# Optimization experiments

Measured on AMD Instinct MI355X. Metric: run time of the kernel, lower is better.

## Reference

```python
import math
import jax, jax.numpy as jnp
import numpy as np

MAX_LEN = 1024

def _sinusoidal_pe(seq_len, d_model):
    pos = jnp.arange(seq_len, dtype=jnp.float32)[:, None]
    div = jnp.exp(jnp.arange(0, d_model, 2, dtype=jnp.float32) * (-math.log(10000.0) / d_model))
    ang = pos * div  # [S, D/2]
    pe = jnp.zeros((seq_len, d_model), dtype=jnp.float32)
    pe = pe.at[:, 0::2].set(jnp.sin(ang))
    pe = pe.at[:, 1::2].set(jnp.cos(ang))
    return pe

def setup_inputs() -> dict:
    key = jax.random.key(0)
    ks = jax.random.split(key, 4)
    B, S, D, H = 4, 1024, 1024, 16
    x = jax.random.normal(ks[0], (B, S, D), dtype=jnp.float32)
    gamma = jnp.ones((D,), dtype=jnp.float32)
    beta = jnp.zeros((D,), dtype=jnp.float32)
    w_pos = jax.random.normal(ks[1], (2 * D, D), dtype=jnp.float32) * (1.0 / math.sqrt(D))
    w_tok = jax.random.normal(ks[2], (3 * D, D), dtype=jnp.float32) * (1.0 / math.sqrt(D))
    bias_table = jax.random.normal(ks[3], (2 * MAX_LEN, H), dtype=jnp.float32) * 0.02
    return {"x": x, "gamma": gamma, "beta": beta, "w_pos": w_pos, "w_tok": w_tok, "bias_table": bias_table}

def reference(x, gamma, beta, w_pos, w_tok, bias_table):
    B, S, D = x.shape
    H = bias_table.shape[1]
    dh = D // H
    scale = 1.0 / math.sqrt(2 * dh)

    # untied positional scores (identical across batch)
    pe = _sinusoidal_pe(S, D)                      # [S, D]
    pos = pe @ w_pos.T                             # [S, 2D]
    pos_k, pos_q = pos[:, :D], pos[:, D:]
    pos_k = pos_k.reshape(S, H, dh)
    pos_q = pos_q.reshape(S, H, dh)
    pos_attn = jnp.einsum('qhd,khd->hqk', pos_q, pos_k)  # [H, S, S]

    # token scores
    mu = jnp.mean(x, axis=-1, keepdims=True)
    var = jnp.mean((x - mu) ** 2, axis=-1, keepdims=True)
    xn = (x - mu) / jnp.sqrt(var + 1e-5) * gamma + beta
    tok = xn @ w_tok.T                             # [B, S, 3D]
    tok_k, tok_q, tok_v = jnp.split(tok, 3, axis=-1)
    tok_k = tok_k.reshape(B, S, H, dh)
    tok_q = tok_q.reshape(B, S, H, dh)
    tok_v = tok_v.reshape(B, S, H, dh)
    tok_attn = jnp.einsum('bqhd,bkhd->bhqk', tok_q, tok_k)  # [B, H, S, S]

    attn = (tok_attn + pos_attn[None]) / scale

    # relative-position bias
    rel = jnp.arange(S)[None, :] - jnp.arange(S)[:, None] + MAX_LEN  # [S, S]
    bias = bias_table[rel]                         # [S, S, H]
    attn = attn + jnp.transpose(bias, (2, 0, 1))[None]

    attn = jax.nn.softmax(attn, axis=-1)
    out = jnp.einsum('bhqk,bkhd->bqhd', attn, tok_v)
    return out.reshape(B, S, D)
```

## Files before the change

kernel.cpp:

```cpp
#include <hip/hip_runtime.h>
#include <math.h>

#define SB 1024
#define DM 1024
#define BB 4
#define NH 16
#define DH 64
#define ML 1024

typedef __attribute__((ext_vector_type(8))) short short8;
typedef __attribute__((ext_vector_type(8))) _Float16 half8;
typedef __attribute__((ext_vector_type(4))) float f32x4;
typedef unsigned short u16;

__device__ __forceinline__ u16 f2bf(float x) {
  unsigned u = __float_as_uint(x);
  u += 0x7fffu + ((u >> 16) & 1u);
  return (u16)(u >> 16);
}
__device__ __forceinline__ float bf2f(u16 h) { return __uint_as_float((unsigned)h << 16); }

__device__ __forceinline__ void async16(void* lds, const void* g) {
  __builtin_amdgcn_global_load_lds(
      (const __attribute__((address_space(1))) unsigned*)g,
      (__attribute__((address_space(3))) unsigned*)lds, 16, 0, 0);
}

#define TPITCH 1028

__global__ __launch_bounds__(256, 4) void prep_all(
    const float* __restrict__ x, const float* __restrict__ gamma,
    const float* __restrict__ beta,
    const float* __restrict__ w_pos, const float* __restrict__ w_tok,
    _Float16* __restrict__ peH, _Float16* __restrict__ peL,
    _Float16* __restrict__ xnH, _Float16* __restrict__ xnL,
    _Float16* __restrict__ wpH, _Float16* __restrict__ wpL,
    _Float16* __restrict__ wtH, _Float16* __restrict__ wtL) {
  __shared__ float T[8 * TPITCH];
  __shared__ float Sred[4][8][2];

  int bid = blockIdx.x, t = threadIdx.x;
  int wv = t >> 6, lane = t & 63;

  int type, rt;
  const float* src = nullptr;
  _Float16 *dH, *dL;
  if (bid < 128)      { type = 0; rt = bid;       dH = peH; dL = peL; }
  else if (bid < 640) { type = 1; rt = bid - 128; src = x;     dH = xnH; dL = xnL; }
  else if (bid < 896) { type = 2; rt = bid - 640; src = w_pos; dH = wpH; dL = wpL; }
  else                { type = 2; rt = bid - 896; src = w_tok; dH = wtH; dL = wtL; }

  if (type == 0) {
    float div0 = exp2f((float)(t * 4)     * (-0.01297628162065376f));
    float div1 = exp2f((float)(t * 4 + 2) * (-0.01297628162065376f));
    #pragma unroll
    for (int i = 0; i < 8; ++i) {
      float p = (float)(rt * 8 + i);
      float a0 = p * div0, a1 = p * div1;
      float4 f;
      f.x = __sinf(a0); f.y = __cosf(a0);
      f.z = __sinf(a1); f.w = __cosf(a1);
      *(float4*)&T[i * TPITCH + t * 4] = f;
    }
  } else if (type == 1) {
    #pragma unroll
    for (int i = 0; i < 8; ++i) {
      float4 f = *(const float4*)(src + (size_t)(rt * 8 + i) * 1024 + t * 4);
      *(float4*)&T[i * TPITCH + t * 4] = f;
    }
  } else {
    #pragma unroll
    for (int i = 0; i < 8; ++i) {
      float4 f = *(const float4*)(src + (size_t)(rt * 8 + i) * 1024 + t * 4);
      f.x *= 32.f; f.y *= 32.f; f.z *= 32.f; f.w *= 32.f;
      *(float4*)&T[i * TPITCH + t * 4] = f;
    }
  }
  __syncthreads();

  if (type == 1) {
    int row = t & 7, cc = t >> 3;
    float s1 = 0.f, s2 = 0.f;
    #pragma unroll
    for (int i = 0; i < 8; ++i) {
      float4 f = *(const float4*)&T[row * TPITCH + cc * 32 + i * 4];
      s1 += f.x + f.y + f.z + f.w;
      s2 += f.x*f.x + f.y*f.y + f.z*f.z + f.w*f.w;
    }
    s1 += __shfl_xor(s1, 8, 64);  s2 += __shfl_xor(s2, 8, 64);
    s1 += __shfl_xor(s1, 16, 64); s2 += __shfl_xor(s2, 16, 64);
    s1 += __shfl_xor(s1, 32, 64); s2 += __shfl_xor(s2, 32, 64);
    if (lane < 8) { Sred[wv][lane][0] = s1; Sred[wv][lane][1] = s2; }
  }
  __syncthreads();

  int row = lane & 7, gg = (lane >> 3) & 3, ktp = lane >> 5;
  float mu = 0.f, rs = 0.f;
  if (type == 1) {
    float s1 = Sred[0][row][0] + Sred[1][row][0] + Sred[2][row][0] + Sred[3][row][0];
    float s2 = Sred[0][row][1] + Sred[1][row][1] + Sred[2][row][1] + Sred[3][row][1];
    mu = s1 * (1.0f / 1024.0f);
    float var = s2 * (1.0f / 1024.0f) - mu * mu;
    rs = rsqrtf(var + 1e-5f);
  }
  int grow16 = rt >> 1;
  int rsub = (rt & 1) * 8 + row;
  #pragma unroll
  for (int q = 0; q < 4; ++q) {
    int kt = wv * 8 + q * 2 + ktp;
    int col = kt * 32 + gg * 8;
    float v[8];
    *(float4*)&v[0] = *(const float4*)&T[row * TPITCH + col];
    *(float4*)&v[4] = *(const float4*)&T[row * TPITCH + col + 4];
    if (type == 1) {
      float4 gp0 = *(const float4*)(gamma + col);
      float4 gp1 = *(const float4*)(gamma + col + 4);
      float4 bp0 = *(const float4*)(beta + col);
      float4 bp1 = *(const float4*)(beta + col + 4);
      v[0] = (v[0]-mu)*rs*gp0.x + bp0.x;  v[1] = (v[1]-mu)*rs*gp0.y + bp0.y;
      v[2] = (v[2]-mu)*rs*gp0.z + bp0.z;  v[3] = (v[3]-mu)*rs*gp0.w + bp0.w;
      v[4] = (v[4]-mu)*rs*gp1.x + bp1.x;  v[5] = (v[5]-mu)*rs*gp1.y + bp1.y;
      v[6] = (v[6]-mu)*rs*gp1.z + bp1.z;  v[7] = (v[7]-mu)*rs*gp1.w + bp1.w;
    }
    half8 hv, lv;
    #pragma unroll
    for (int j = 0; j < 8; ++j) {
      _Float16 h = (_Float16)v[j];
      hv[j] = h;
      lv[j] = (_Float16)(v[j] - (float)h);
    }
    size_t off = ((size_t)(grow16 * 32 + kt) * 64 + rsub + gg * 16) * 8;
    *(half8*)(dH + off) = hv;
    *(half8*)(dL + off) = lv;
  }
}

__global__ __launch_bounds__(256, 2) void gemm16p(
    const _Float16* __restrict__ AtH, const _Float16* __restrict__ AtL,
    const _Float16* __restrict__ ApH, const _Float16* __restrict__ ApL,
    const _Float16* __restrict__ BtH, const _Float16* __restrict__ BtL,
    const _Float16* __restrict__ BpH, const _Float16* __restrict__ BpL,
    u16* __restrict__ KtfH, u16* __restrict__ KtfL,
    u16* __restrict__ KpfH, u16* __restrict__ KpfL,
    u16* __restrict__ QH, u16* __restrict__ QL,
    u16* __restrict__ pQH, u16* __restrict__ pQL,
    u16* __restrict__ vF, float sK, float sQ, float sV) {
  __shared__ _Float16 L[32 * 512];
  int t = threadIdx.x;
  int wv = t >> 6, lane = t & 63;
  int wm = wv >> 1, wn = wv & 1;
  int r16 = lane & 15, g = lane >> 4;

  int phys = blockIdx.x;
  int bid = (phys & 7) * 56 + (phys >> 3);
  bool isPos = (bid >= 384);
  int idx = isPos ? bid - 384 : bid;
  int n0, m0;
  const _Float16 *AH, *AL, *BH, *BL;
  if (isPos) { n0 = (idx & 7) * 256;  m0 = (idx >> 3) * 128;
               AH = ApH; AL = ApL; BH = BpH; BL = BpL; }
  else       { n0 = (idx % 12) * 256; m0 = (idx / 12) * 128;
               AH = AtH; AL = AtL; BH = BtH; BL = BtL; }
  int mt0 = m0 >> 4, nt0 = n0 >> 4;
  bool split = isPos || (n0 < 2048);

  f32x4 acc[4][8];
  #pragma unroll
  for (int i = 0; i < 4; ++i)
    #pragma unroll
    for (int j = 0; j < 8; ++j) acc[i][j] = (f32x4){0.f, 0.f, 0.f, 0.f};

  for (int kt = 0; kt < 32; ++kt) {
    __syncthreads();
    #pragma unroll
    for (int rd = 0; rd < 8; ++rd) {
      int ci = rd * 4 + wv;
      bool isAlo = (ci < 16) && (ci & 1);
      if (!split && isAlo) continue;
      const _Float16* src;
      if (ci < 16) {
        int mt = ci >> 1, pl = ci & 1;
        const _Float16* P = pl ? AL : AH;
        src = P + ((size_t)((mt0 + mt) * 32 + kt) * 64 + lane) * 8;
      } else {
        int nt = ci - 16;
        src = BH + ((size_t)((nt0 + nt) * 32 + kt) * 64 + lane) * 8;
      }
      async16(&L[ci * 512], src);
    }
    half8 blo[8];
    if (split) {
      #pragma unroll
      for (int j = 0; j < 8; ++j) {
        int ntg = nt0 + wn * 8 + j;
        blo[j] = *(const half8*)(BL + ((size_t)(ntg * 32 + kt) * 64 + lane) * 8);
      }
    }
    __syncthreads();

    half8 ah[4], al[4];
    #pragma unroll
    for (int i = 0; i < 4; ++i)
      ah[i] = *(const half8*)&L[(((wm * 4 + i) * 2 + 0) * 512) + lane * 8];
    if (split) {
      #pragma unroll
      for (int i = 0; i < 4; ++i)
        al[i] = *(const half8*)&L[(((wm * 4 + i) * 2 + 1) * 512) + lane * 8];
    }
    #pragma unroll
    for (int j = 0; j < 8; ++j) {
      half8 bh = *(const half8*)&L[((16 + wn * 8 + j) * 512) + lane * 8];
      #pragma unroll
      for (int i = 0; i < 4; ++i) {
        acc[i][j] = __builtin_amdgcn_mfma_f32_16x16x32_f16(ah[i], bh, acc[i][j], 0, 0, 0);
        if (split) {
          acc[i][j] = __builtin_amdgcn_mfma_f32_16x16x32_f16(al[i], bh, acc[i][j], 0, 0, 0);
          acc[i][j] = __builtin_amdgcn_mfma_f32_16x16x32_f16(ah[i], blo[j], acc[i][j], 0, 0, 0);
        }
      }
    }
  }

  int band = n0 >> 10;
  u16* fKH = isPos ? KpfH : KtfH;
  u16* fKL = isPos ? KpfL : KtfL;
  u16* qHo = isPos ? pQH  : QH;
  u16* qLo = isPos ? pQL  : QL;
  if (band == 1) {
    #pragma unroll
    for (int i = 0; i < 4; ++i)
      #pragma unroll
      for (int j = 0; j < 8; ++j) {
        int lc = (n0 & 1023) + wn * 128 + j * 16 + r16;
        #pragma unroll
        for (int reg = 0; reg < 4; ++reg) {
          int row = m0 + wm * 64 + i * 16 + g * 4 + reg;
          float cv = acc[i][j][reg] * sQ;
          u16 hi = f2bf(cv);
          qHo[(size_t)row * 1024 + lc] = hi;
          qLo[(size_t)row * 1024 + lc] = f2bf(cv - bf2f(hi));
        }
      }
  } else if (band == 0) {
    #pragma unroll
    for (int i = 0; i < 4; ++i)
      #pragma unroll
      for (int j = 0; j < 8; ++j) {
        int colg = n0 + wn * 128 + j * 16 + r16;
        int h = colg >> 6, dc = colg & 63;
        #pragma unroll
        for (int reg = 0; reg < 4; ++reg) {
          int row = m0 + wm * 64 + i * 16 + g * 4 + reg;
          int bhK = (row >> 10) * NH + h;
          size_t a = ((size_t)((bhK * 64 + ((row & 1023) >> 4)) * 2 + (dc >> 5)) << 9)
                   + ((row & 15) + 16 * ((dc >> 3) & 3)) * 8 + (dc & 7);
          float cv = acc[i][j][reg] * sK;
          u16 hi = f2bf(cv);
          fKH[a] = hi;
          fKL[a] = f2bf(cv - bf2f(hi));
        }
      }
  } else {
    #pragma unroll
    for (int i = 0; i < 4; ++i)
      #pragma unroll
      for (int j = 0; j < 8; ++j) {
        int colg = (n0 & 1023) + wn * 128 + j * 16 + r16;
        int h = colg >> 6, dc = colg & 63;
        #pragma unroll
        for (int reg = 0; reg < 4; ++reg) {
          int row = m0 + wm * 64 + i * 16 + g * 4 + reg;
          int s = row & 1023;
          size_t a = ((size_t)((((row >> 10) * NH + h) * 32 + (s >> 5)) * 4 + (dc >> 4)) << 9)
                   + ((s >> 3) & 3) * 128 + (s & 7) + (dc & 15) * 8;
          vF[a] = f2bf(acc[i][j][reg] * sV);
        }
      }
  }
}

__global__ __launch_bounds__(256, 2) void gemm16m(
    const _Float16* __restrict__ AtH, const _Float16* __restrict__ AtL,
    const _Float16* __restrict__ ApH, const _Float16* __restrict__ ApL,
    const float* __restrict__ Wt, const float* __restrict__ Wp,
    u16* __restrict__ KtfH, u16* __restrict__ KtfL,
    u16* __restrict__ KpfH, u16* __restrict__ KpfL,
    u16* __restrict__ QH, u16* __restrict__ QL,
    u16* __restrict__ pQH, u16* __restrict__ pQL,
    u16* __restrict__ vF, float sK, float sQ, float sV) {
  __shared__ _Float16 L[48 * 512];
  int t = threadIdx.x;
  int wv = t >> 6, lane = t & 63;
  int wm = wv >> 1, wn = wv & 1;
  int r16 = lane & 15, g = lane >> 4;

  int phys = blockIdx.x;
  int bid = (phys & 7) * 56 + (phys >> 3);
  bool isPos = (bid >= 384);
  int idx = isPos ? bid - 384 : bid;
  int n0, m0;
  const _Float16 *AH, *AL;
  const float* W;
  if (isPos) { n0 = (idx & 7) * 256;  m0 = (idx >> 3) * 128; AH = ApH; AL = ApL; W = Wp; }
  else       { n0 = (idx % 12) * 256; m0 = (idx / 12) * 128; AH = AtH; AL = AtL; W = Wt; }
  int mt0 = m0 >> 4, nt0 = n0 >> 4;
  bool split = isPos || (n0 < 2048);

  f32x4 acc[4][8];
  #pragma unroll
  for (int i = 0; i < 4; ++i)
    #pragma unroll
    for (int j = 0; j < 8; ++j) acc[i][j] = (f32x4){0.f, 0.f, 0.f, 0.f};

  for (int kt = 0; kt < 32; ++kt) {
    __syncthreads();
    #pragma unroll
    for (int rd = 0; rd < 4; ++rd) {
      int ci = rd * 4 + wv;
      int mt = ci >> 1, pl = ci & 1;
      if (!split && pl) continue;
      const _Float16* src = (pl ? AL : AH)
          + ((size_t)((mt0 + mt) * 32 + kt) * 64 + lane) * 8;
      async16(&L[ci * 512], src);
    }
    #pragma unroll
    for (int tt = 0; tt < 4; ++tt) {
      int nt = wv * 4 + tt;
      const float* wsrc = W + (size_t)((nt0 + nt) * 16 + r16) * 1024 + kt * 32 + g * 8;
      float4 w0 = *(const float4*)wsrc;
      float4 w1 = *(const float4*)(wsrc + 4);
      float wvv[8] = {w0.x, w0.y, w0.z, w0.w, w1.x, w1.y, w1.z, w1.w};
      half8 hv, lv;
      #pragma unroll
      for (int j = 0; j < 8; ++j) {
        float xx = wvv[j] * 32.0f;
        _Float16 h = (_Float16)xx;
        hv[j] = h;
        lv[j] = (_Float16)(xx - (float)h);
      }
      *(half8*)&L[(16 + nt) * 512 + lane * 8] = hv;
      if (split) *(half8*)&L[(32 + nt) * 512 + lane * 8] = lv;
    }
    __syncthreads();

    half8 ah[4], al[4];
    #pragma unroll
    for (int i = 0; i < 4; ++i)
      ah[i] = *(const half8*)&L[(((wm * 4 + i) * 2 + 0) * 512) + lane * 8];
    if (split) {
      #pragma unroll
      for (int i = 0; i < 4; ++i)
        al[i] = *(const half8*)&L[(((wm * 4 + i) * 2 + 1) * 512) + lane * 8];
    }
    #pragma unroll
    for (int j = 0; j < 8; ++j) {
      half8 bh = *(const half8*)&L[((16 + wn * 8 + j) * 512) + lane * 8];
      #pragma unroll
      for (int i = 0; i < 4; ++i) {
        acc[i][j] = __builtin_amdgcn_mfma_f32_16x16x32_f16(ah[i], bh, acc[i][j], 0, 0, 0);
        if (split) {
          half8 bl = *(const half8*)&L[((32 + wn * 8 + j) * 512) + lane * 8];
          acc[i][j] = __builtin_amdgcn_mfma_f32_16x16x32_f16(al[i], bh, acc[i][j], 0, 0, 0);
          acc[i][j] = __builtin_amdgcn_mfma_f32_16x16x32_f16(ah[i], bl, acc[i][j], 0, 0, 0);
        }
      }
    }
  }

  int band = n0 >> 10;
  u16* fKH = isPos ? KpfH : KtfH;
  u16* fKL = isPos ? KpfL : KtfL;
  u16* qHo = isPos ? pQH  : QH;
  u16* qLo = isPos ? pQL  : QL;
  if (band == 1) {
    #pragma unroll
    for (int i = 0; i < 4; ++i)
      #pragma unroll
      for (int j = 0; j < 8; ++j) {
        int lc = (n0 & 1023) + wn * 128 + j * 16 + r16;
        #pragma unroll
        for (int reg = 0; reg < 4; ++reg) {
          int row = m0 + wm * 64 + i * 16 + g * 4 + reg;
          float cv = acc[i][j][reg] * sQ;
          u16 hi = f2bf(cv);
          qHo[(size_t)row * 1024 + lc] = hi;
          qLo[(size_t)row * 1024 + lc] = f2bf(cv - bf2f(hi));
        }
      }
  } else if (band == 0) {
    #pragma unroll
    for (int i = 0; i < 4; ++i)
      #pragma unroll
      for (int j = 0; j < 8; ++j) {
        int colg = n0 + wn * 128 + j * 16 + r16;
        int h = colg >> 6, dc = colg & 63;
        #pragma unroll
        for (int reg = 0; reg < 4; ++reg) {
          int row = m0 + wm * 64 + i * 16 + g * 4 + reg;
          int bhK = (row >> 10) * NH + h;
          size_t a = ((size_t)((bhK * 64 + ((row & 1023) >> 4)) * 2 + (dc >> 5)) << 9)
                   + ((row & 15) + 16 * ((dc >> 3) & 3)) * 8 + (dc & 7);
          float cv = acc[i][j][reg] * sK;
          u16 hi = f2bf(cv);
          fKH[a] = hi;
          fKL[a] = f2bf(cv - bf2f(hi));
        }
      }
  } else {
    #pragma unroll
    for (int i = 0; i < 4; ++i)
      #pragma unroll
      for (int j = 0; j < 8; ++j) {
        int colg = (n0 & 1023) + wn * 128 + j * 16 + r16;
        int h = colg >> 6, dc = colg & 63;
        #pragma unroll
        for (int reg = 0; reg < 4; ++reg) {
          int row = m0 + wm * 64 + i * 16 + g * 4 + reg;
          int s = row & 1023;
          size_t a = ((size_t)((((row >> 10) * NH + h) * 32 + (s >> 5)) * 4 + (dc >> 4)) << 9)
                   + ((s >> 3) & 3) * 128 + (s & 7) + (dc & 15) * 8;
          vF[a] = f2bf(acc[i][j][reg] * sV);
        }
      }
  }
}

__global__ __launch_bounds__(256, 2) void attn_mfma10(
    const u16* __restrict__ KtfH, const u16* __restrict__ KtfL,
    const u16* __restrict__ KpfH, const u16* __restrict__ KpfL,
    const u16* __restrict__ QHg, const u16* __restrict__ QLg,
    const u16* __restrict__ pQH, const u16* __restrict__ pQL,
    const u16* __restrict__ Vf,
    const float* __restrict__ bt,
    float* __restrict__ out) {
  __shared__ u16 Klds[5 * 4096];
  __shared__ float biasL[2 * ML];
  __shared__ u16 Pb[4][16 * 72];

  int phys = blockIdx.x;
  int bid = (phys & 7) * 64 + (phys >> 3);
  int qt = bid & 7;
  int bh = bid >> 3;
  int b = bh >> 4, h = bh & 15;
  int q0 = qt * 128;
  int t = threadIdx.x;
  int wv = t >> 6, lane = t & 63;
  int g = lane >> 4, r16 = lane & 15;
  int lo = lane * 8;

  #pragma unroll
  for (int k = 0; k < 8; ++k)
    biasL[t + k * 256] = bt[(size_t)(t + k * 256) * NH + h];

  short8 qhi[2][4], qlo[2][4];
  #pragma unroll
  for (int cc = 0; cc < 2; ++cc) {
    int qrow = q0 + wv * 32 + cc * 16 + r16;
    #pragma unroll
    for (int c = 0; c < 4; ++c) {
      if (c < 2) {
        size_t off = (size_t)(b * SB + qrow) * 1024 + h * DH + c * 32 + g * 8;
        qhi[cc][c] = *(const short8*)(QHg + off);
        qlo[cc][c] = *(const short8*)(QLg + off);
      } else {
        size_t off = (size_t)qrow * 1024 + h * DH + (c - 2) * 32 + g * 8;
        qhi[cc][c] = *(const short8*)(pQH + off);
        qlo[cc][c] = *(const short8*)(pQL + off);
      }
    }
  }

  f32x4 O[2][4];
  #pragma unroll
  for (int cc = 0; cc < 2; ++cc)
    #pragma unroll
    for (int dt = 0; dt < 4; ++dt) O[cc][dt] = (f32x4){0.f, 0.f, 0.f, 0.f};
  float m_run[2][4], l_run[2][4];
  #pragma unroll
  for (int cc = 0; cc < 2; ++cc)
    #pragma unroll
    for (int reg = 0; reg < 4; ++reg) { m_run[cc][reg] = -3e38f; l_run[cc][reg] = 0.f; }

  int qb0 = q0 + wv * 32 + g * 4;
  const u16* ktHb = KtfH + (size_t)(bh * 64) * 1024;
  const u16* ktLb = KtfL + (size_t)(bh * 64) * 1024;
  const u16* kpHb = KpfH + (size_t)(h * 64) * 1024;
  const u16* kpLb = KpfL + (size_t)(h * 64) * 1024;
  const u16* vb   = Vf   + (size_t)(bh * 32) * 2048;
  int bb = ML + r16 - qb0;

  for (int ktr = 0; ktr < 16; ++ktr) {
    __syncthreads();

    {
      int p0 = wv * 512, p1 = (wv + 4) * 512;
      async16(&Klds[0 * 4096 + p0], ktHb + p0 + lo);
      async16(&Klds[0 * 4096 + p1], ktHb + p1 + lo);
      async16(&Klds[1 * 4096 + p0], ktLb + p0 + lo);
      async16(&Klds[1 * 4096 + p1], ktLb + p1 + lo);
      async16(&Klds[2 * 4096 + p0], kpHb + p0 + lo);
      async16(&Klds[2 * 4096 + p1], kpHb + p1 + lo);
      async16(&Klds[3 * 4096 + p0], kpLb + p0 + lo);
      async16(&Klds[3 * 4096 + p1], kpLb + p1 + lo);
      async16(&Klds[4 * 4096 + p0], vb + p0 + lo);
      async16(&Klds[4 * 4096 + p1], vb + p1 + lo);
    }

    float bias[2][4][4];
    #pragma unroll
    for (int nt = 0; nt < 4; ++nt)
      #pragma unroll
      for (int reg = 0; reg < 4; ++reg) {
        bias[0][nt][reg] = biasL[bb + nt * 16 - reg];
        bias[1][nt][reg] = biasL[bb - 16 + nt * 16 - reg];
      }

    asm volatile("s_waitcnt vmcnt(0)" ::: "memory");
    __syncthreads();

    f32x4 S[2][4];
    #pragma unroll
    for (int nt = 0; nt < 4; ++nt) {
      f32x4 a0 = (f32x4){0.f, 0.f, 0.f, 0.f};
      f32x4 a1 = (f32x4){0.f, 0.f, 0.f, 0.f};
      #pragma unroll
      for (int c = 0; c < 4; ++c) {
        int ch = (c < 2) ? 0 : 2;
        int co = c & 1;
        short8 bhi = *(const short8*)&Klds[(ch + 0) * 4096 + nt * 1024 + co * 512 + lo];
        short8 blo = *(const short8*)&Klds[(ch + 1) * 4096 + nt * 1024 + co * 512 + lo];
        a0 = __builtin_amdgcn_mfma_f32_16x16x32_bf16(qhi[0][c], bhi, a0, 0, 0, 0);
        a1 = __builtin_amdgcn_mfma_f32_16x16x32_bf16(qhi[1][c], bhi, a1, 0, 0, 0);
        a0 = __builtin_amdgcn_mfma_f32_16x16x32_bf16(qlo[0][c], bhi, a0, 0, 0, 0);
        a1 = __builtin_amdgcn_mfma_f32_16x16x32_bf16(qlo[1][c], bhi, a1, 0, 0, 0);
        a0 = __builtin_amdgcn_mfma_f32_16x16x32_bf16(qhi[0][c], blo, a0, 0, 0, 0);
        a1 = __builtin_amdgcn_mfma_f32_16x16x32_bf16(qhi[1][c], blo, a1, 0, 0, 0);
      }
      S[0][nt] = a0; S[1][nt] = a1;
    }

    short8 vfrag[2][4];
    #pragma unroll
    for (int kc = 0; kc < 2; ++kc)
      #pragma unroll
      for (int dt = 0; dt < 4; ++dt)
        vfrag[kc][dt] = *(const short8*)&Klds[4 * 4096 + (kc * 4 + dt) * 512 + lo];

    #pragma unroll
    for (int cc = 0; cc < 2; ++cc)
      #pragma unroll
      for (int nt = 0; nt < 4; ++nt)
        #pragma unroll
        for (int reg = 0; reg < 4; ++reg)
          S[cc][nt][reg] += bias[cc][nt][reg];

    float tm[2][4], al[2][4];
    #pragma unroll
    for (int cc = 0; cc < 2; ++cc)
      #pragma unroll
      for (int reg = 0; reg < 4; ++reg)
        tm[cc][reg] = fmaxf(fmaxf(S[cc][0][reg], S[cc][1][reg]),
                            fmaxf(S[cc][2][reg], S[cc][3][reg]));
    #pragma unroll
    for (int off = 1; off < 16; off <<= 1)
      #pragma unroll
      for (int cc = 0; cc < 2; ++cc)
        #pragma unroll
        for (int reg = 0; reg < 4; ++reg)
          tm[cc][reg] = fmaxf(tm[cc][reg], __shfl_xor(tm[cc][reg], off, 64));
    #pragma unroll
    for (int cc = 0; cc < 2; ++cc)
      #pragma unroll
      for (int reg = 0; reg < 4; ++reg) {
        float mn = fmaxf(m_run[cc][reg], tm[cc][reg]);
        al[cc][reg] = __expf(m_run[cc][reg] - mn);
        m_run[cc][reg] = mn;
      }
    float ts[2][4] = {{0.f, 0.f, 0.f, 0.f}, {0.f, 0.f, 0.f, 0.f}};
    #pragma unroll
    for (int cc = 0; cc < 2; ++cc)
      #pragma unroll
      for (int nt = 0; nt < 4; ++nt)
        #pragma unroll
        for (int reg = 0; reg < 4; ++reg) {
          float p = __expf(S[cc][nt][reg] - m_run[cc][reg]);
          S[cc][nt][reg] = p;
          ts[cc][reg] += p;
        }
    #pragma unroll
    for (int cc = 0; cc < 2; ++cc)
      #pragma unroll
      for (int reg = 0; reg < 4; ++reg)
        l_run[cc][reg] = l_run[cc][reg] * al[cc][reg] + ts[cc][reg];
    #pragma unroll
    for (int cc = 0; cc < 2; ++cc)
      #pragma unroll
      for (int dt = 0; dt < 4; ++dt)
        #pragma unroll
        for (int reg = 0; reg < 4; ++reg)
          O[cc][dt][reg] *= al[cc][reg];

    #pragma unroll
    for (int cc = 0; cc < 2; ++cc) {
      u16* pb = Pb[wv];
      #pragma unroll
      for (int nt = 0; nt < 4; ++nt)
        #pragma unroll
        for (int reg = 0; reg < 4; ++reg)
          pb[(g * 4 + reg) * 72 + nt * 16 + r16] = f2bf(S[cc][nt][reg]);
      #pragma unroll
      for (int kc = 0; kc < 2; ++kc) {
        short8 pa = *(const short8*)&Pb[wv][r16 * 72 + kc * 32 + g * 8];
        #pragma unroll
        for (int dt = 0; dt < 4; ++dt)
          O[cc][dt] = __builtin_amdgcn_mfma_f32_16x16x32_bf16(pa, vfrag[kc][dt], O[cc][dt], 0, 0, 0);
      }
    }

    ktHb += 4096; ktLb += 4096; kpHb += 4096; kpLb += 4096;
    vb += 4096; bb += 64;
  }

  #pragma unroll
  for (int off = 1; off < 16; off <<= 1)
    #pragma unroll
    for (int cc = 0; cc < 2; ++cc)
      #pragma unroll
      for (int reg = 0; reg < 4; ++reg)
        l_run[cc][reg] += __shfl_xor(l_run[cc][reg], off, 64);
  #pragma unroll
  for (int cc = 0; cc < 2; ++cc)
    #pragma unroll
    for (int reg = 0; reg < 4; ++reg) l_run[cc][reg] = 1.0f / l_run[cc][reg];
  #pragma unroll
  for (int cc = 0; cc < 2; ++cc)
    #pragma unroll
    for (int dt = 0; dt < 4; ++dt)
      #pragma unroll
      for (int reg = 0; reg < 4; ++reg)
        out[(size_t)(b * SB + qb0 + cc * 16 + reg) * DM + h * DH + dt * 16 + r16] =
            O[cc][dt][reg] * l_run[cc][reg];
}

extern "C" void kernel_launch(void* const* d_in, const int* in_sizes, int n_in,
                              void* d_out, int out_size, void* d_ws, size_t ws_size,
                              hipStream_t stream) {
  const float* x     = (const float*)d_in[0];
  const float* gamma = (const float*)d_in[1];
  const float* beta  = (const float*)d_in[2];
  const float* w_pos = (const float*)d_in[3];
  const float* w_tok = (const float*)d_in[4];
  const float* bt    = (const float*)d_in[5];
  float* out = (float*)d_out;
  float* ws  = (float*)d_ws;
  const size_t M1 = 1u << 20;
  const float IS = 11.313708498984761f;

  u16 *KtfH, *KtfL, *KpfH, *KpfL, *QH, *QL, *posQH, *posQL, *Vf;

  if (ws_size >= 22 * M1 * 4) {
    _Float16* peH = (_Float16*)(ws);
    _Float16* peL = (_Float16*)(ws + M1 / 2);
    _Float16* xnH = (_Float16*)(ws + 1 * M1);
    _Float16* xnL = (_Float16*)(ws + 3 * M1);
    _Float16* wpH = (_Float16*)(ws + 5 * M1);
    _Float16* wpL = (_Float16*)(ws + 6 * M1);
    _Float16* wtH = (_Float16*)(ws + 7 * M1);
    _Float16* wtL = (_Float16*)(ws + 8 * M1 + M1/2);
    KpfH  = (u16*)(ws + 10 * M1);
    KpfL  = (u16*)(ws + 10 * M1 + M1 / 2);
    posQH = (u16*)(ws + 11 * M1);
    posQL = (u16*)(ws + 11 * M1 + M1 / 2);
    KtfH  = (u16*)(ws + 12 * M1);
    KtfL  = (u16*)(ws + 14 * M1);
    QH    = (u16*)(ws + 16 * M1);
    QL    = (u16*)(ws + 18 * M1);
    Vf    = (u16*)(ws + 20 * M1);

    prep_all<<<1280, 256, 0, stream>>>(x, gamma, beta, w_pos, w_tok,
        peH, peL, xnH, xnL, wpH, wpL, wtH, wtL);
    gemm16p<<<448, 256, 0, stream>>>(
        xnH, xnL, peH, peL, wtH, wtL, wpH, wpL,
        KtfH, KtfL, KpfH, KpfL, QH, QL, posQH, posQL, Vf,
        1.0f / 32.0f, IS / 32.0f, 1.0f / 32.0f);
  } else {
    _Float16* peH = (_Float16*)(ws);
    _Float16* peL = (_Float16*)(ws + M1 / 2);
    _Float16* xnH = (_Float16*)(ws + 1 * M1);
    _Float16* xnL = (_Float16*)(ws + 3 * M1);
    KpfH  = (u16*)(ws + 5 * M1);
    KpfL  = (u16*)(ws + 5 * M1 + M1 / 2);
    posQH = (u16*)(ws + 6 * M1);
    posQL = (u16*)(ws + 6 * M1 + M1 / 2);
    KtfH  = (u16*)(ws + 7 * M1);
    KtfL  = (u16*)(ws + 9 * M1);
    QH    = (u16*)(ws + 11 * M1);
    QL    = (u16*)(ws + 13 * M1);
    Vf    = (u16*)(ws + 15 * M1);

    prep_all<<<640, 256, 0, stream>>>(x, gamma, beta, w_pos, w_tok,
        peH, peL, xnH, xnL, (_Float16*)nullptr, (_Float16*)nullptr,
        (_Float16*)nullptr, (_Float16*)nullptr);
    gemm16m<<<448, 256, 0, stream>>>(
        xnH, xnL, peH, peL, w_tok, w_pos,
        KtfH, KtfL, KpfH, KpfL, QH, QL, posQH, posQL, Vf,
        1.0f / 32.0f, IS / 32.0f, 1.0f / 32.0f);
  }

  attn_mfma10<<<BB * NH * (SB / 128), 256, 0, stream>>>(
      KtfH, KtfL, KpfH, KpfL, QH, QL, posQH, posQL, Vf, bt, out);
}
```

Before: 244.2 us.

## Double-buffer K/V tiles in LDS and read positional K directly from global

The attention kernel now double-buffers the token-K hi/lo and V tiles in LDS. The next tile's async loads are issued right after the barrier, so they overlap the current tile's MFMA and softmax work, and the second barrier per iteration is gone. Positional K tiles, which are shared across the batch, are no longer staged through LDS and are read straight from global memory, relying on cache hits. Part of the bias values are reused between the two row groups, so fewer bias values are read from LDS. The risk is that global-latency loads for positional K now sit on the MFMA critical path, and total LDS use grows slightly.

```diff
diff --git a/kernel.cpp b/kernel.cpp
--- a/kernel.cpp
+++ b/kernel.cpp
@@ -12,6 +12,10 @@
 typedef __attribute__((ext_vector_type(8))) _Float16 half8;
 typedef __attribute__((ext_vector_type(4))) float f32x4;
 typedef unsigned short u16;
+
+#define S_BARRIER() __builtin_amdgcn_s_barrier()
+#define SCHED_FENCE() __builtin_amdgcn_sched_barrier(0)
+#define WAITVL() asm volatile("s_waitcnt vmcnt(0) lgkmcnt(0)" ::: "memory")
 
 __device__ __forceinline__ u16 f2bf(float x) {
   unsigned u = __float_as_uint(x);
@@ -425,7 +429,18 @@
   }
 }
 
-__global__ __launch_bounds__(256, 2) void attn_mfma10(
+__device__ __forceinline__ void stage_tv(u16* B,
+    const u16* ktH, const u16* ktL, const u16* vb, int wv, int lo) {
+  int p0 = wv * 512, p1 = (wv + 4) * 512;
+  async16(&B[0 * 4096 + p0], ktH + p0 + lo);
+  async16(&B[0 * 4096 + p1], ktH + p1 + lo);
+  async16(&B[1 * 4096 + p0], ktL + p0 + lo);
+  async16(&B[1 * 4096 + p1], ktL + p1 + lo);
+  async16(&B[2 * 4096 + p0], vb + p0 + lo);
+  async16(&B[2 * 4096 + p1], vb + p1 + lo);
+}
+
+__global__ __launch_bounds__(256, 2) void attn_mfma12(
     const u16* __restrict__ KtfH, const u16* __restrict__ KtfL,
     const u16* __restrict__ KpfH, const u16* __restrict__ KpfL,
     const u16* __restrict__ QHg, const u16* __restrict__ QLg,
@@ -433,7 +448,7 @@
     const u16* __restrict__ Vf,
     const float* __restrict__ bt,
     float* __restrict__ out) {
-  __shared__ u16 Klds[5 * 4096];
+  __shared__ u16 Klds[2][3 * 4096];
   __shared__ float biasL[2 * ML];
   __shared__ u16 Pb[4][16 * 72];
 
@@ -484,39 +499,30 @@
   int qb0 = q0 + wv * 32 + g * 4;
   const u16* ktHb = KtfH + (size_t)(bh * 64) * 1024;
   const u16* ktLb = KtfL + (size_t)(bh * 64) * 1024;
-  const u16* kpHb = KpfH + (size_t)(h * 64) * 1024;
-  const u16* kpLb = KpfL + (size_t)(h * 64) * 1024;
+  const u16* kpHb = KpfH + (size_t)(h * 64) * 1024 + lo;
+  const u16* kpLb = KpfL + (size_t)(h * 64) * 1024 + lo;
   const u16* vb   = Vf   + (size_t)(bh * 32) * 2048;
   int bb = ML + r16 - qb0;
 
+  stage_tv(&Klds[0][0], ktHb, ktLb, vb, wv, lo);
+
   for (int ktr = 0; ktr < 16; ++ktr) {
-    __syncthreads();
-
-    {
-      int p0 = wv * 512, p1 = (wv + 4) * 512;
-      async16(&Klds[0 * 4096 + p0], ktHb + p0 + lo);
-      async16(&Klds[0 * 4096 + p1], ktHb + p1 + lo);
-      async16(&Klds[1 * 4096 + p0], ktLb + p0 + lo);
-      async16(&Klds[1 * 4096 + p1], ktLb + p1 + lo);
-      async16(&Klds[2 * 4096 + p0], kpHb + p0 + lo);
-      async16(&Klds[2 * 4096 + p1], kpHb + p1 + lo);
-      async16(&Klds[3 * 4096 + p0], kpLb + p0 + lo);
-      async16(&Klds[3 * 4096 + p1], kpLb + p1 + lo);
-      async16(&Klds[4 * 4096 + p0], vb + p0 + lo);
-      async16(&Klds[4 * 4096 + p1], vb + p1 + lo);
-    }
-
-    float bias[2][4][4];
+    u16* buf = &Klds[ktr & 1][0];
+    WAITVL();
+    S_BARRIER();
+    SCHED_FENCE();
+    if (ktr < 15)
+      stage_tv(&Klds[(ktr + 1) & 1][0], ktHb + 4096, ktLb + 4096, vb + 4096, wv, lo);
+
+    float bias0[4][4], bias1[4];
     #pragma unroll
     for (int nt = 0; nt < 4; ++nt)
       #pragma unroll
-      for (int reg = 0; reg < 4; ++reg) {
-        bias[0][nt][reg] = biasL[bb + nt * 16 - reg];
-        bias[1][nt][reg] = biasL[bb - 16 + nt * 16 - reg];
-      }
-
-    asm volatile("s_waitcnt vmcnt(0)" ::: "memory");
-    __syncthreads();
+      for (int reg = 0; reg < 4; ++reg)
+        bias0[nt][reg] = biasL[bb + nt * 16 - reg];
+    #pragma unroll
+    for (int reg = 0; reg < 4; ++reg)
+      bias1[reg] = biasL[bb - 16 - reg];
 
     f32x4 S[2][4];
     #pragma unroll
@@ -525,10 +531,15 @@
       f32x4 a1 = (f32x4){0.f, 0.f, 0.f, 0.f};
       #pragma unroll
       for (int c = 0; c < 4; ++c) {
-        int ch = (c < 2) ? 0 : 2;
         int co = c & 1;
-        short8 bhi = *(const short8*)&Klds[(ch + 0) * 4096 + nt * 1024 + co * 512 + lo];
-        short8 blo = *(const short8*)&Klds[(ch + 1) * 4096 + nt * 1024 + co * 512 + lo];
+        short8 bhi, blo;
+        if (c < 2) {
+          bhi = *(const short8*)&buf[0 * 4096 + nt * 1024 + co * 512 + lo];
+          blo = *(const short8*)&buf[1 * 4096 + nt * 1024 + co * 512 + lo];
+        } else {
+          bhi = *(const short8*)(kpHb + nt * 1024 + co * 512);
+          blo = *(const short8*)(kpLb + nt * 1024 + co * 512);
+        }
         a0 = __builtin_amdgcn_mfma_f32_16x16x32_bf16(qhi[0][c], bhi, a0, 0, 0, 0);
         a1 = __builtin_amdgcn_mfma_f32_16x16x32_bf16(qhi[1][c], bhi, a1, 0, 0, 0);
         a0 = __builtin_amdgcn_mfma_f32_16x16x32_bf16(qlo[0][c], bhi, a0, 0, 0, 0);
@@ -544,15 +555,15 @@
     for (int kc = 0; kc < 2; ++kc)
       #pragma unroll
       for (int dt = 0; dt < 4; ++dt)
-        vfrag[kc][dt] = *(const short8*)&Klds[4 * 4096 + (kc * 4 + dt) * 512 + lo];
-
-    #pragma unroll
-    for (int cc = 0; cc < 2; ++cc)
-      #pragma unroll
-      for (int nt = 0; nt < 4; ++nt)
-        #pragma unroll
-        for (int reg = 0; reg < 4; ++reg)
-          S[cc][nt][reg] += bias[cc][nt][reg];
+        vfrag[kc][dt] = *(const short8*)&buf[2 * 4096 + (kc * 4 + dt) * 512 + lo];
+
+    #pragma unroll
+    for (int nt = 0; nt < 4; ++nt)
+      #pragma unroll
+      for (int reg = 0; reg < 4; ++reg) {
+        S[0][nt][reg] += bias0[nt][reg];
+        S[1][nt][reg] += (nt == 0) ? bias1[reg] : bias0[nt - 1][reg];
+      }
 
     float tm[2][4], al[2][4];
     #pragma unroll
@@ -707,6 +718,6 @@
         1.0f / 32.0f, IS / 32.0f, 1.0f / 32.0f);
   }
 
-  attn_mfma10<<<BB * NH * (SB / 128), 256, 0, stream>>>(
+  attn_mfma12<<<BB * NH * (SB / 128), 256, 0, stream>>>(
       KtfH, KtfL, KpfH, KpfL, QH, QL, posQH, posQL, Vf, bt, out);
 }
```

New measurement: 253.1 us. 3.6% more time.
